# Performance work log

Hardware: AMD Instinct MI355X
Metric: run time of the kernel (lower is better)

## Reference

```python
import jax, jax.numpy as jnp
import numpy as np
import math

T, B = 512, 32
QD, SD, H, NH = 128, 256, 512, 8
NQ, NS, NSUB = 30000, 400, 8
DKEY = QD + 2 * SD      # 640
DVAL = 4 * SD + QD      # 1152
P = H + 2 * SD + QD     # 1152 (pred_in_feature)
DH = H // NH            # 64
NEG = -1e32


def _layernorm(x, g, b, eps=1e-5):
    mu = jnp.mean(x, axis=-1, keepdims=True)
    var = jnp.mean((x - mu) ** 2, axis=-1, keepdims=True)
    return (x - mu) * jax.lax.rsqrt(var + eps) * g + b


def setup_inputs() -> dict:
    key = jax.random.key(0)
    ks = iter(jax.random.split(key, 48))
    def nrm(shape, scale=0.05):
        return (scale * jax.random.normal(next(ks), shape)).astype(jnp.float32)
    inp = {}
    inp['ans'] = jax.random.randint(next(ks), (T, B), 1, 5, dtype=jnp.int32)
    inp['correct_ans'] = jax.random.randint(next(ks), (T, B), 1, 5, dtype=jnp.int32)
    inp['labels'] = jax.random.randint(next(ks), (T, B), 0, 2, dtype=jnp.int32)
    inp['mask'] = jnp.ones((T, B), jnp.float32)
    inp['q_ids'] = jax.random.randint(next(ks), (T, B), 0, NQ, dtype=jnp.int32)
    inp['subject_ids'] = jax.random.randint(next(ks), (T, B, NSUB), 0, NS, dtype=jnp.int32)
    inp['subject_mask'] = (jax.random.uniform(next(ks), (T, B, NSUB)) < 0.7).astype(jnp.float32)
    inp['Eq'] = nrm((NQ, QD)); inp['Es'] = nrm((NS, SD))
    inp['Ea'] = nrm((4, SD)); inp['El'] = nrm((2, SD))
    inp['Wq'] = nrm((H, DKEY)); inp['bq'] = jnp.zeros((H,), jnp.float32)
    inp['Wk'] = nrm((H, DKEY)); inp['bk'] = jnp.zeros((H,), jnp.float32)
    inp['Wv'] = nrm((H, DVAL)); inp['bv'] = jnp.zeros((H,), jnp.float32)
    inp['Wo'] = nrm((H, H)); inp['bo'] = jnp.zeros((H,), jnp.float32)
    inp['ln1_g'] = jnp.ones((H,), jnp.float32); inp['ln1_b'] = jnp.zeros((H,), jnp.float32)
    inp['W1'] = nrm((H, H)); inp['b1'] = jnp.zeros((H,), jnp.float32)
    inp['W2'] = nrm((H, H)); inp['b2'] = jnp.zeros((H,), jnp.float32)
    inp['ln2_g'] = jnp.ones((H,), jnp.float32); inp['ln2_b'] = jnp.zeros((H,), jnp.float32)
    inp['gammas'] = jnp.zeros((NH, 1, 1), jnp.float32)
    inp['L1W'] = nrm((P, P)); inp['L1b'] = jnp.zeros((P,), jnp.float32)
    inp['L2W'] = nrm((P, P)); inp['L2b'] = jnp.zeros((P,), jnp.float32)
    inp['OW'] = nrm((1, P)); inp['Ob'] = jnp.zeros((1,), jnp.float32)
    return inp


def _forward(ans, correct_ans, labels, q_ids, subject_ids,
             mask, subject_mask, Eq, Es, Ea, El,
             Wq, bq, Wk, bk, Wv, bv, Wo, bo, ln1_g, ln1_b,
             W1, b1, W2, b2, ln2_g, ln2_b, gammas,
             L1W, L1b, L2W, L2b, OW, Ob):
    m3 = mask[:, :, None]                                   # [T,B,1]
    subjects = jnp.sum(Es[subject_ids] * subject_mask[..., None], axis=2)   # [T,B,SD]
    questions = Eq[q_ids]                                   # [T,B,QD]
    ans_embed = Ea[ans - 1] * m3
    ca_embed = Ea[correct_ans - 1]
    lab_embed = El[labels] * m3
    query = jnp.concatenate([questions, subjects, ca_embed], axis=-1)       # [T,B,DKEY]
    value = jnp.concatenate([lab_embed, ans_embed, ca_embed, questions, subjects], axis=-1)  # [T,B,DVAL]
    # note: original applies q_linear to kk and k_linear to qq (qq==kk==query here); akt=True => no pos-embed
    q = (query @ Wq.T + bq).reshape(T, B, NH, DH).transpose(1, 2, 0, 3)     # [B,NH,T,DH]
    k = (query @ Wk.T + bk).reshape(T, B, NH, DH).transpose(1, 2, 0, 3)
    v = (value @ Wv.T + bv).reshape(T, B, NH, DH).transpose(1, 2, 0, 3)
    scores = jnp.einsum('bhqd,bhkd->bhqk', q, k) / math.sqrt(DH)            # [B,NH,T,T]
    scores = jnp.where(mask.T[:, None, None, :] == 0, NEG, scores)
    # exponential distance decay (Softplus-gamma), applied AFTER the key-pad fill as in the original
    idx = jnp.arange(T)
    pe = jnp.sqrt(jnp.abs(idx[None, :] - idx[:, None]).astype(jnp.float32)) # [T,T]
    total_effect = jnp.clip(jnp.exp(pe[None] * (-jax.nn.softplus(gammas))), 1e-5, 1e5)  # [NH,T,T]
    scores = scores * total_effect[None]
    causal_bad = jnp.triu(jnp.ones((T, T), bool))            # upper incl. diagonal is masked
    scores = jnp.where(causal_bad, NEG, scores)
    scores = jax.nn.softmax(scores, axis=-1)
    scores = scores.at[:, :, 0, :].set(0.0)                  # pad-zero first query row
    attn = jnp.einsum('bhqk,bhkd->bhqd', scores, v)
    concat = attn.transpose(2, 0, 1, 3).reshape(T, B, H)
    out = _layernorm(concat @ Wo.T + bo, ln1_g, ln1_b)
    ffn = jax.nn.relu(out @ W1.T + b1) @ W2.T + b2
    out = out + _layernorm(ffn, ln2_g, ln2_b)
    pred = jnp.concatenate([out, questions, subjects, ca_embed], axis=-1)   # [T,B,P]
    h = jax.nn.relu(pred @ L1W.T + L1b)
    h = jax.nn.relu(h @ L2W.T + L2b)
    logits = ((h + pred) @ OW.T + Ob)[..., 0]                # [T,B]
    y = labels.astype(jnp.float32)
    bce = jnp.maximum(logits, 0.0) - logits * y + jnp.log1p(jnp.exp(-jnp.abs(logits)))
    loss = jnp.mean(bce * mask) / jnp.mean(mask)
    return loss


def reference(ans, correct_ans, labels, mask, q_ids, subject_ids, subject_mask,
              Eq, Es, Ea, El, Wq, bq, Wk, bk, Wv, bv, Wo, bo, ln1_g, ln1_b,
              W1, b1, W2, b2, ln2_g, ln2_b, gammas, L1W, L1b, L2W, L2b, OW, Ob):
    return _forward(ans, correct_ans, labels, q_ids, subject_ids,
                    mask, subject_mask, Eq, Es, Ea, El,
                    Wq, bq, Wk, bk, Wv, bv, Wo, bo, ln1_g, ln1_b,
                    W1, b1, W2, b2, ln2_g, ln2_b, gammas,
                    L1W, L1b, L2W, L2b, OW, Ob)
```

## Files before the change

kernel.cpp:

```cpp
#include <hip/hip_runtime.h>
#include <math.h>

#define T_LEN 512
#define B_SZ  32
#define NHEAD 8
#define DHEAD 64
#define H_DIM 512
#define TBTOK 16384
#define P_DIM 1152

typedef unsigned short ushort_t;
typedef short short8 __attribute__((ext_vector_type(8)));
typedef float f32x4 __attribute__((ext_vector_type(4)));

__device__ __forceinline__ ushort_t f2bf(float f) {
    union { float f; unsigned int u; } v; v.f = f;
    unsigned int r = v.u + 0x7fffu + ((v.u >> 16) & 1u);
    return (ushort_t)(r >> 16);
}
__device__ __forceinline__ float bf2f(ushort_t h) {
    union { unsigned int u; float f; } v; v.u = ((unsigned int)h) << 16;
    return v.f;
}
__device__ __forceinline__ void gload_lds16(const void* g, void* l) {
    __builtin_amdgcn_global_load_lds(
        (const __attribute__((address_space(1))) void*)g,
        (__attribute__((address_space(3))) void*)l, 16, 0, 0);
}

__global__ __launch_bounds__(256) void convert_weights(
    const float* __restrict__ wq, const float* __restrict__ wk,
    const float* __restrict__ wv, const float* __restrict__ wo,
    const float* __restrict__ w1, const float* __restrict__ w2,
    const float* __restrict__ l1, const float* __restrict__ l2,
    ushort_t* __restrict__ dst)
{
    const unsigned int offs[9] = {0u, 327680u, 655360u, 1245184u, 1507328u,
                                  1769472u, 2031616u, 3358720u, 4685824u};
    unsigned int c = (blockIdx.x * 256 + threadIdx.x) * 4;
    const float* srcs[8] = {wq, wk, wv, wo, w1, w2, l1, l2};
    int s = 0;
#pragma unroll
    for (int i = 0; i < 7; i++) s += (c >= offs[i + 1]) ? 1 : 0;
    float4 v = *(const float4*)(srcs[s] + (c - offs[s]));
    ushort4 o;
    o.x = f2bf(v.x); o.y = f2bf(v.y); o.z = f2bf(v.z); o.w = f2bf(v.w);
    *(ushort4*)(dst + c) = o;
}

__global__ __launch_bounds__(256) void embed_kernel(
    const int* __restrict__ ans, const int* __restrict__ cans,
    const int* __restrict__ labels, const float* __restrict__ mask,
    const int* __restrict__ qids, const int* __restrict__ sids,
    const float* __restrict__ smask,
    const float* __restrict__ Eq, const float* __restrict__ Es,
    const float* __restrict__ Ea, const float* __restrict__ El,
    ushort_t* __restrict__ pred_bf, ushort_t* __restrict__ value_bf)
{
    int m = blockIdx.x;
    int tid = threadIdx.x;
    float mval = mask[m];
    int qid = qids[m];
    int a   = ans[m] - 1;
    int ca  = cans[m] - 1;
    int lb  = labels[m];
    ushort_t* pr = pred_bf  + (size_t)m * P_DIM;
    ushort_t* vr = value_bf + (size_t)m * P_DIM;

    if (tid < 128) {
        ushort_t qv = f2bf(Eq[(size_t)qid * 128 + tid]);
        pr[512 + tid] = qv;
        vr[768 + tid] = qv;
    }
    int d = tid;
    float s = 0.f;
#pragma unroll
    for (int j = 0; j < 8; j++) {
        int  sid = sids[m * 8 + j];
        float sm = smask[m * 8 + j];
        s += Es[(size_t)sid * 256 + d] * sm;
    }
    ushort_t sb = f2bf(s);
    pr[640 + d] = sb;
    vr[896 + d] = sb;
    ushort_t cab = f2bf(Ea[ca * 256 + d]);
    pr[896 + d] = cab;
    vr[512 + d] = cab;
    vr[256 + d] = f2bf(Ea[a * 256 + d] * mval);
    vr[0   + d] = f2bf(El[lb * 256 + d] * mval);
}

template<int MODE, bool RELU>
__global__ __launch_bounds__(256) void mgemm(
    const ushort_t* __restrict__ A, int lda,
    const ushort_t* __restrict__ W, int ldw,
    const float* __restrict__ bias, const float* __restrict__ bias2,
    ushort_t* __restrict__ Cb, ushort_t* __restrict__ Cb2, int ldc, int K,
    const float* __restrict__ OW, float* __restrict__ lg)
{
    __shared__ __align__(16) ushort_t As[128 * 32];
    __shared__ __align__(16) ushort_t Ws[128 * 32];
    __shared__ __align__(16) ushort_t et[4][32][72];

    const int m0 = blockIdx.x * 128;
    const int n0 = blockIdx.y * 128;
    const int tid  = threadIdx.x;
    const int wave = tid >> 6;
    const int lane = tid & 63;
    const int wm = wave & 1, wn = wave >> 1;

    f32x4 acc[4][4] = {};

    const int srow = lane >> 2;
    const int lchunk = ((((lane & 3) - ((srow >> 1) & 3)) & 3)) * 8;
    int arowA, arowB;
    if (MODE == 4) {
        int mA = m0 + wave * 32 + srow;
        int mB = mA + 16;
        arowA = ((mA & 511) << 5) + (mA >> 9);
        arowB = ((mB & 511) << 5) + (mB >> 9);
    } else {
        arowA = m0 + wave * 32 + srow;
        arowB = arowA + 16;
    }
    const ushort_t* Ag0 = A + (size_t)arowA * lda + lchunk;
    const ushort_t* Ag1 = A + (size_t)arowB * lda + lchunk;
    const ushort_t* Wg0 = W + (size_t)(n0 + wave * 32 + srow) * ldw + lchunk;
    const ushort_t* Wg1 = Wg0 + (size_t)16 * ldw;
    ushort_t* Al0 = &As[(wave * 32) * 32];
    ushort_t* Al1 = &As[(wave * 32 + 16) * 32];
    ushort_t* Wl0 = &Ws[(wave * 32) * 32];
    ushort_t* Wl1 = &Ws[(wave * 32 + 16) * 32];

    const int fr   = lane & 15;
    const int quad = lane >> 4;
    const int csw  = ((quad + ((fr >> 1) & 3)) & 3) * 8;

    for (int k0 = 0; k0 < K; k0 += 32) {
        gload_lds16(Ag0 + k0, Al0);
        gload_lds16(Ag1 + k0, Al1);
        gload_lds16(Wg0 + k0, Wl0);
        gload_lds16(Wg1 + k0, Wl1);
        __syncthreads();
        short8 af[4], wf[4];
#pragma unroll
        for (int i = 0; i < 4; i++)
            af[i] = *(const short8*)&As[(wm * 64 + i * 16 + fr) * 32 + csw];
#pragma unroll
        for (int j = 0; j < 4; j++)
            wf[j] = *(const short8*)&Ws[(wn * 64 + j * 16 + fr) * 32 + csw];
#pragma unroll
        for (int i = 0; i < 4; i++)
#pragma unroll
            for (int j = 0; j < 4; j++)
                acc[i][j] = __builtin_amdgcn_mfma_f32_16x16x32_bf16(
                    af[i], wf[j], acc[i][j], 0, 0, 0);
        __syncthreads();
    }

    if (MODE == 3) {
#pragma unroll
        for (int i = 0; i < 4; i++)
#pragma unroll
            for (int r = 0; r < 4; r++) {
                int row = m0 + wm * 64 + i * 16 + quad * 4 + r;
                float part = 0.f;
#pragma unroll
                for (int j = 0; j < 4; j++) {
                    int col = n0 + wn * 64 + j * 16 + fr;
                    float v = fmaxf(acc[i][j][r] + bias[col], 0.f);
                    part = fmaf(v, OW[col], part);
                }
                part += __shfl_xor(part, 1, 64);
                part += __shfl_xor(part, 2, 64);
                part += __shfl_xor(part, 4, 64);
                part += __shfl_xor(part, 8, 64);
                if (fr == 0) atomicAdd(&lg[row], part);
            }
        return;
    }

    const int nbase = n0 + wn * 64;
    bool side = (MODE == 5) && (nbase >= 512);
    const float* bp = side ? bias2 : bias;
    const int boff  = (MODE == 5) ? (nbase & 511) : nbase;
    const float scl = (MODE == 5 && !side) ? 0.125f : 1.f;

    const int sub8 = (lane & 7) * 8;
    const int grp  = lane >> 3;

#pragma unroll
    for (int hh = 0; hh < 2; hh++) {
        if (MODE == 4) {
#pragma unroll
            for (int i = 0; i < 4; i++)
#pragma unroll
                for (int r = 0; r < 4; r++) {
                    int rl = i * 16 + quad * 4 + r;
#pragma unroll
                    for (int j = 2 * hh; j < 2 * hh + 2; j++) {
                        int cl = j * 16 + fr;
                        float v = acc[i][j][r] + bp[boff + cl];
                        if (RELU) v = fmaxf(v, 0.f);
                        et[wave][cl - 32 * hh][rl] = f2bf(v);
                    }
                }
        } else {
#pragma unroll
            for (int i = 2 * hh; i < 2 * hh + 2; i++)
#pragma unroll
                for (int r = 0; r < 4; r++) {
                    int rl = i * 16 + quad * 4 + r;
#pragma unroll
                    for (int j = 0; j < 4; j++) {
                        int cl = j * 16 + fr;
                        float v = (acc[i][j][r] + bp[boff + cl]) * scl;
                        if (RELU) v = fmaxf(v, 0.f);
                        et[wave][rl - 32 * hh][cl] = f2bf(v);
                    }
                }
        }
#pragma unroll
        for (int rr = 0; rr < 4; rr++) {
            int rowl = rr * 8 + grp;
            short8 val = *(const short8*)&et[wave][rowl][sub8];
            if (MODE == 1) {
                int row = m0 + wm * 64 + 32 * hh + rowl;
                int col = nbase + sub8;
                *(short8*)&Cb[(size_t)row * ldc + col] = val;
            } else if (MODE == 5) {
                int row = m0 + wm * 64 + 32 * hh + rowl;
                int t = row >> 5, b = row & 31;
                int h = (nbase >> 6) & 7;
                ushort_t* base = side ? Cb2 : Cb;
                *(short8*)&base[(((size_t)(b * 8 + h)) << 15) + ((size_t)t << 6) + sub8] = val;
            } else {
                int m = m0 + wm * 64 + sub8;
                int b = m >> 9, t = m & 511;
                int h = nbase >> 6;
                int d = 32 * hh + rowl;
                *(short8*)&Cb[(((size_t)(b * 8 + h)) << 15) + ((size_t)d << 9) + t] = val;
            }
        }
    }
}

__global__ __launch_bounds__(256) void attn_mfma(
    const ushort_t* __restrict__ qb, const ushort_t* __restrict__ kb,
    const ushort_t* __restrict__ vtb, const float* __restrict__ mask,
    const float* __restrict__ gammas, ushort_t* __restrict__ attnc)
{
    __shared__ __align__(16) ushort_t kbuf[2][64 * 64];
    __shared__ __align__(16) ushort_t vbuf[2][64 * 64];
    __shared__ __align__(16) ushort_t ps[4][16][72];
    __shared__ float decayF[512];
    __shared__ float mneg[512];

    const int bh  = blockIdx.x;
    const int b   = bh >> 3;
    const int h   = bh & 7;
    const int qt0 = (7 - blockIdx.y) * 64;
    const int tid  = threadIdx.x;
    const int wave = tid >> 6;
    const int lane = tid & 63;
    const int fr   = lane & 15;
    const int quad = lane >> 4;

    {
        float g  = gammas[h];
        float sp = (g > 20.f) ? g : log1pf(expf(g));
        for (int i = tid; i < 512; i += 256) {
            decayF[i] = fmaxf(exp2f(-sp * 1.44269504f * sqrtf((float)i)), 1e-5f)
                        * 1.44269504f;
            mneg[i]   = (mask[(size_t)i * B_SZ + b] == 0.f) ? -1e32f : 0.f;
        }
    }

    const int qr0 = qt0 + wave * 16;
    const ushort_t* qbase = qb  + ((size_t)bh << 15);
    const ushort_t* kbase = kb  + ((size_t)bh << 15);
    const ushort_t* vbase = vtb + ((size_t)bh << 15);

    short8 af0 = *(const short8*)(qbase + (size_t)(qr0 + fr) * 64 + quad * 8);
    short8 af1 = *(const short8*)(qbase + (size_t)(qr0 + fr) * 64 + 32 + quad * 8);
    const short8 ones = {0x3F80, 0x3F80, 0x3F80, 0x3F80,
                         0x3F80, 0x3F80, 0x3F80, 0x3F80};

    const int rl0 = wave * 16 + (lane >> 3);
    const int rl1 = rl0 + 8;
    const int sc0 = (((lane & 7) - rl0) & 7) * 8;
    const int sc1 = (((lane & 7) - rl1) & 7) * 8;

    auto stage = [&](int kt, int bufi) {
        gload_lds16(kbase + (size_t)(kt + rl0) * 64 + sc0, &kbuf[bufi][(wave * 16) * 64]);
        gload_lds16(kbase + (size_t)(kt + rl1) * 64 + sc1, &kbuf[bufi][(wave * 16 + 8) * 64]);
        gload_lds16(vbase + (size_t)rl0 * T_LEN + kt + sc0, &vbuf[bufi][(wave * 16) * 64]);
        gload_lds16(vbase + (size_t)rl1 * T_LEN + kt + sc1, &vbuf[bufi][(wave * 16 + 8) * 64]);
    };
    auto frag = [&](const ushort_t* buf, int row, int lchunk) -> short8 {
        return *(const short8*)&buf[row * 64 + ((lchunk + row) & 7) * 8];
    };

    stage(0, 0);

    f32x4 o[4] = {};
    f32x4 lacc = {};
    int bufi = 0;

    for (int kt0 = 0; kt0 <= qt0; kt0 += 64) {
        __syncthreads();
        if (kt0 < qt0) stage(kt0 + 64, bufi ^ 1);
        const bool diag = (kt0 == qt0);
        const ushort_t* kb_ = kbuf[bufi];
        const ushort_t* vb_ = vbuf[bufi];

        f32x4 sacc[4] = {};
#pragma unroll
        for (int j = 0; j < 4; j++) {
            int row = j * 16 + fr;
            short8 k0 = frag(kb_, row, quad);
            short8 k1 = frag(kb_, row, quad + 4);
            sacc[j] = __builtin_amdgcn_mfma_f32_16x16x32_bf16(af0, k0, sacc[j], 0, 0, 0);
            sacc[j] = __builtin_amdgcn_mfma_f32_16x16x32_bf16(af1, k1, sacc[j], 0, 0, 0);
        }

#pragma unroll
        for (int j = 0; j < 4; j++) {
            int kg = kt0 + j * 16 + fr;
            float mn = mneg[kg];
            int qgb = qr0 + quad * 4;
            if (!diag) {
                int base = qgb - kg;
#pragma unroll
                for (int r = 0; r < 4; r++) {
                    float t = fmaf(sacc[j][r], decayF[base + r], mn);
                    union { float f; unsigned u; } cv; cv.f = exp2f(t);
                    ps[wave][quad * 4 + r][j * 16 + fr] = (ushort_t)(cv.u >> 16);
                }
            } else {
#pragma unroll
                for (int r = 0; r < 4; r++) {
                    int didx = qgb + r - kg;
                    float dec = decayF[didx > 0 ? didx : 0];
                    float t = fmaf(sacc[j][r], dec, mn);
                    if (didx <= 0) t = -1e32f;
                    union { float f; unsigned u; } cv; cv.f = exp2f(t);
                    ps[wave][quad * 4 + r][j * 16 + fr] = (ushort_t)(cv.u >> 16);
                }
            }
        }
        short8 pf0 = *(const short8*)&ps[wave][fr][quad * 8];
        short8 pf1 = *(const short8*)&ps[wave][fr][32 + quad * 8];
        lacc = __builtin_amdgcn_mfma_f32_16x16x32_bf16(pf0, ones, lacc, 0, 0, 0);
        lacc = __builtin_amdgcn_mfma_f32_16x16x32_bf16(pf1, ones, lacc, 0, 0, 0);
#pragma unroll
        for (int j2 = 0; j2 < 4; j2++) {
            int row = j2 * 16 + fr;
            short8 v0 = frag(vb_, row, quad);
            short8 v1 = frag(vb_, row, quad + 4);
            o[j2] = __builtin_amdgcn_mfma_f32_16x16x32_bf16(pf0, v0, o[j2], 0, 0, 0);
            o[j2] = __builtin_amdgcn_mfma_f32_16x16x32_bf16(pf1, v1, o[j2], 0, 0, 0);
        }
        bufi ^= 1;
    }

#pragma unroll
    for (int r = 0; r < 4; r++) {
        int qg = qr0 + quad * 4 + r;
        float linv = (qg == 0) ? 0.f : 1.f / lacc[r];
#pragma unroll
        for (int j2 = 0; j2 < 4; j2++)
            ps[wave][quad * 4 + r][j2 * 16 + fr] = f2bf(o[j2][r] * linv);
    }
    const int sub8 = (lane & 7) * 8;
    const int grp  = lane >> 3;
#pragma unroll
    for (int half = 0; half < 2; half++) {
        int rowl = half * 8 + grp;
        short8 val = *(const short8*)&ps[wave][rowl][sub8];
        int qg = qr0 + rowl;
        *(short8*)&attnc[((size_t)qg * B_SZ + b) * H_DIM + h * DHEAD + sub8] = val;
    }
}

__global__ __launch_bounds__(256) void ln1_kernel(
    const ushort_t* __restrict__ X, const float* __restrict__ g,
    const float* __restrict__ bta, float* __restrict__ Y,
    ushort_t* __restrict__ Yb)
{
    int m    = blockIdx.x * 4 + (threadIdx.x >> 6);
    int lane = threadIdx.x & 63;
    int c0   = lane * 8;
    const ushort_t* xr = X + (size_t)m * H_DIM + c0;
    float x[8];
    float s = 0.f, ss = 0.f;
    short8 xv = *(const short8*)xr;
#pragma unroll
    for (int i = 0; i < 8; i++) {
        x[i] = bf2f((ushort_t)xv[i]);
        s += x[i]; ss += x[i] * x[i];
    }
#pragma unroll
    for (int off = 32; off >= 1; off >>= 1) {
        s  += __shfl_xor(s,  off, 64);
        ss += __shfl_xor(ss, off, 64);
    }
    float mu  = s * (1.f / 512.f);
    float var = ss * (1.f / 512.f) - mu * mu;
    float rs  = rsqrtf(var + 1e-5f);
    float  yo[8];
    ushort_t yb[8];
#pragma unroll
    for (int i = 0; i < 8; i++) {
        float v = (x[i] - mu) * rs * g[c0 + i] + bta[c0 + i];
        yo[i] = v; yb[i] = f2bf(v);
    }
    *(float4*)(Y + (size_t)m * H_DIM + c0)     = *(float4*)&yo[0];
    *(float4*)(Y + (size_t)m * H_DIM + c0 + 4) = *(float4*)&yo[4];
    *(short8*)(Yb + (size_t)m * H_DIM + c0)    = *(short8*)&yb[0];
}

__global__ __launch_bounds__(256) void ln2_kernel(
    const ushort_t* __restrict__ X, const float* __restrict__ g,
    const float* __restrict__ bta, const float* __restrict__ res,
    ushort_t* __restrict__ pred_bf, const float* __restrict__ OW,
    float* __restrict__ lg)
{
    int m    = blockIdx.x * 4 + (threadIdx.x >> 6);
    int lane = threadIdx.x & 63;
    int c0   = lane * 8;
    const ushort_t* xr = X + (size_t)m * H_DIM + c0;
    float x[8];
    float s = 0.f, ss = 0.f;
    short8 xv = *(const short8*)xr;
#pragma unroll
    for (int i = 0; i < 8; i++) {
        x[i] = bf2f((ushort_t)xv[i]);
        s += x[i]; ss += x[i] * x[i];
    }
#pragma unroll
    for (int off = 32; off >= 1; off >>= 1) {
        s  += __shfl_xor(s,  off, 64);
        ss += __shfl_xor(ss, off, 64);
    }
    float mu  = s * (1.f / 512.f);
    float var = ss * (1.f / 512.f) - mu * mu;
    float rs  = rsqrtf(var + 1e-5f);
    float4 r0 = *(const float4*)(res + (size_t)m * H_DIM + c0);
    float4 r1 = *(const float4*)(res + (size_t)m * H_DIM + c0 + 4);
    float rr[8] = {r0.x, r0.y, r0.z, r0.w, r1.x, r1.y, r1.z, r1.w};
    ushort_t yb[8];
    float part = 0.f;
#pragma unroll
    for (int i = 0; i < 8; i++) {
        float v = (x[i] - mu) * rs * g[c0 + i] + bta[c0 + i] + rr[i];
        yb[i] = f2bf(v);
        part = fmaf(v, OW[c0 + i], part);
    }
    *(short8*)(pred_bf + (size_t)m * P_DIM + c0) = *(short8*)&yb[0];
#pragma unroll
    for (int off = 32; off >= 1; off >>= 1) part += __shfl_xor(part, off, 64);
    if (lane == 0) lg[m] += part;
}

__global__ __launch_bounds__(256) void predot_early(
    const ushort_t* __restrict__ pred_bf, const float* __restrict__ OW,
    const float* __restrict__ Ob, float* __restrict__ lg,
    float* __restrict__ accum)
{
    if (blockIdx.x == 0 && threadIdx.x < 2) accum[threadIdx.x] = 0.f;
    int m    = blockIdx.x * 4 + (threadIdx.x >> 6);
    int lane = threadIdx.x & 63;
    const ushort_t* pr = pred_bf + (size_t)m * P_DIM;
    float s = 0.f;
#pragma unroll 5
    for (int c = 512 + lane; c < P_DIM; c += 64)
        s = fmaf(bf2f(pr[c]), OW[c], s);
#pragma unroll
    for (int off = 32; off >= 1; off >>= 1) s += __shfl_xor(s, off, 64);
    if (lane == 0) lg[m] = s + Ob[0];
}

__global__ __launch_bounds__(256) void bce_kernel(
    const float* __restrict__ lg, const int* __restrict__ labels,
    const float* __restrict__ mask, float* __restrict__ accum)
{
    int m    = blockIdx.x * 256 + threadIdx.x;
    int lane = threadIdx.x & 63;
    float l  = lg[m];
    float y  = (float)labels[m];
    float mv = mask[m];
    float a  = (fmaxf(l, 0.f) - l * y + log1pf(expf(-fabsf(l)))) * mv;
#pragma unroll
    for (int off = 32; off >= 1; off >>= 1) {
        a  += __shfl_xor(a,  off, 64);
        mv += __shfl_xor(mv, off, 64);
    }
    if (lane == 0) {
        atomicAdd(accum,     a);
        atomicAdd(accum + 1, mv);
    }
}

__global__ void finalize_kernel(const float* __restrict__ accum, float* __restrict__ out)
{
    out[0] = accum[0] / accum[1];
}

extern "C" void kernel_launch(void* const* d_in, const int* in_sizes, int n_in,
                              void* d_out, int out_size, void* d_ws, size_t ws_size,
                              hipStream_t stream)
{
    (void)in_sizes; (void)n_in; (void)out_size;
    const int*   ans    = (const int*)  d_in[0];
    const int*   cans   = (const int*)  d_in[1];
    const int*   labels = (const int*)  d_in[2];
    const float* mask   = (const float*)d_in[3];
    const int*   qids   = (const int*)  d_in[4];
    const int*   sids   = (const int*)  d_in[5];
    const float* smask  = (const float*)d_in[6];
    const float* Eq     = (const float*)d_in[7];
    const float* Es     = (const float*)d_in[8];
    const float* Ea     = (const float*)d_in[9];
    const float* El     = (const float*)d_in[10];
    const float* Wq     = (const float*)d_in[11];
    const float* bq     = (const float*)d_in[12];
    const float* Wk     = (const float*)d_in[13];
    const float* bk     = (const float*)d_in[14];
    const float* Wv     = (const float*)d_in[15];
    const float* bv     = (const float*)d_in[16];
    const float* Wo     = (const float*)d_in[17];
    const float* bo     = (const float*)d_in[18];
    const float* ln1_g  = (const float*)d_in[19];
    const float* ln1_b  = (const float*)d_in[20];
    const float* W1     = (const float*)d_in[21];
    const float* b1     = (const float*)d_in[22];
    const float* W2     = (const float*)d_in[23];
    const float* b2     = (const float*)d_in[24];
    const float* ln2_g  = (const float*)d_in[25];
    const float* ln2_b  = (const float*)d_in[26];
    const float* gammas = (const float*)d_in[27];
    const float* L1W    = (const float*)d_in[28];
    const float* L1b    = (const float*)d_in[29];
    const float* L2W    = (const float*)d_in[30];
    const float* L2b    = (const float*)d_in[31];
    const float* OW     = (const float*)d_in[32];
    const float* Ob     = (const float*)d_in[33];
    float* out = (float*)d_out;

    const size_t U = (size_t)TBTOK * 64;
    if (ws_size < 42 * U * sizeof(float)) return;
    float* ws = (float*)d_ws;
    ushort_t* wtb      = (ushort_t*)(ws);
    ushort_t* pred_bf  = (ushort_t*)(ws + 3 * U);
    ushort_t* value_bf = (ushort_t*)(ws + 12 * U);
    ushort_t* qb       = (ushort_t*)(ws + 21 * U);
    ushort_t* kb       = (ushort_t*)(ws + 25 * U);
    ushort_t* vtb      = (ushort_t*)(ws + 29 * U);
    ushort_t* attnc_bf = (ushort_t*)(ws + 33 * U);
    ushort_t* x1_bf    = (ushort_t*)(ws + 12 * U);
    float*    out1     = ws + 16 * U;
    ushort_t* out1_bf  = (ushort_t*)(ws + 24 * U);
    ushort_t* f1_bf    = (ushort_t*)(ws + 28 * U);
    ushort_t* f2_bf    = (ushort_t*)(ws + 32 * U);
    ushort_t* h1_bf    = (ushort_t*)(ws + 12 * U);
    float*    lgits    = ws + 41 * U;
    float*    accum    = lgits + TBTOK;

    ushort_t* wqk_b = wtb + 0;
    ushort_t* wv_b  = wtb + 655360;
    ushort_t* wo_b  = wtb + 1245184;
    ushort_t* w1_b  = wtb + 1507328;
    ushort_t* w2_b  = wtb + 1769472;
    ushort_t* l1_b  = wtb + 2031616;
    ushort_t* l2_b  = wtb + 3358720;

    convert_weights<<<4576, 256, 0, stream>>>(Wq, Wk, Wv, Wo, W1, W2, L1W, L2W, wtb);
    embed_kernel<<<TBTOK, 256, 0, stream>>>(ans, cans, labels, mask, qids, sids,
                                            smask, Eq, Es, Ea, El, pred_bf, value_bf);
    predot_early<<<TBTOK/4, 256, 0, stream>>>(pred_bf, OW, Ob, lgits, accum);
    mgemm<5,false><<<dim3(TBTOK/128, 8), 256, 0, stream>>>(
        pred_bf + 512, P_DIM, wqk_b, 640, bq, bk, qb, kb, 0, 640, nullptr, nullptr);
    mgemm<4,false><<<dim3(TBTOK/128, 4), 256, 0, stream>>>(
        value_bf, P_DIM, wv_b, P_DIM, bv, nullptr, vtb, nullptr, 0, P_DIM, nullptr, nullptr);
    attn_mfma<<<dim3(B_SZ * NHEAD, 8), 256, 0, stream>>>(
        qb, kb, vtb, mask, gammas, attnc_bf);
    mgemm<1,false><<<dim3(TBTOK/128, 4), 256, 0, stream>>>(
        attnc_bf, H_DIM, wo_b, H_DIM, bo, nullptr, x1_bf, nullptr, H_DIM, H_DIM, nullptr, nullptr);
    ln1_kernel<<<TBTOK/4, 256, 0, stream>>>(x1_bf, ln1_g, ln1_b, out1, out1_bf);
    mgemm<1,true><<<dim3(TBTOK/128, 4), 256, 0, stream>>>(
        out1_bf, H_DIM, w1_b, H_DIM, b1, nullptr, f1_bf, nullptr, H_DIM, H_DIM, nullptr, nullptr);
    mgemm<1,false><<<dim3(TBTOK/128, 4), 256, 0, stream>>>(
        f1_bf, H_DIM, w2_b, H_DIM, b2, nullptr, f2_bf, nullptr, H_DIM, H_DIM, nullptr, nullptr);
    ln2_kernel<<<TBTOK/4, 256, 0, stream>>>(f2_bf, ln2_g, ln2_b, out1, pred_bf, OW, lgits);
    mgemm<1,true><<<dim3(TBTOK/128, 9), 256, 0, stream>>>(
        pred_bf, P_DIM, l1_b, P_DIM, L1b, nullptr, h1_bf, nullptr, P_DIM, P_DIM, nullptr, nullptr);
    mgemm<3,true><<<dim3(TBTOK/128, 9), 256, 0, stream>>>(
        h1_bf, P_DIM, l2_b, P_DIM, L2b, nullptr, nullptr, nullptr, 0, P_DIM, OW, lgits);
    bce_kernel<<<TBTOK/256, 256, 0, stream>>>(lgits, labels, mask, accum);
    finalize_kernel<<<1, 1, 0, stream>>>(accum, out);
}
```

Baseline: 485.0 us.

## Fuse pred logit dot into embed kernel and alias mgemm epilogue LDS

Removes the separate predot_early kernel by computing the pred columns 512..1151 dot with OW inside embed_kernel via wave shuffles and an LDS reduction, and moves accum zeroing into convert_weights. Separately, mgemm's epilogue staging buffer now aliases the A/W tile LDS and writes in four 16-row passes instead of two 32-row passes, cutting shared memory per block to raise occupancy. This saves one launch and a re-read of pred_bf, but adds a __syncthreads to the embed kernel and more epilogue iterations.

```diff
diff --git a/kernel.cpp b/kernel.cpp
--- a/kernel.cpp
+++ b/kernel.cpp
@@ -33,8 +33,9 @@
     const float* __restrict__ wv, const float* __restrict__ wo,
     const float* __restrict__ w1, const float* __restrict__ w2,
     const float* __restrict__ l1, const float* __restrict__ l2,
-    ushort_t* __restrict__ dst)
-{
+    ushort_t* __restrict__ dst, float* __restrict__ accum)
+{
+    if (blockIdx.x == 0 && threadIdx.x < 2) accum[threadIdx.x] = 0.f;
     const unsigned int offs[9] = {0u, 327680u, 655360u, 1245184u, 1507328u,
                                   1769472u, 2031616u, 3358720u, 4685824u};
     unsigned int c = (blockIdx.x * 256 + threadIdx.x) * 4;
@@ -55,8 +56,11 @@
     const float* __restrict__ smask,
     const float* __restrict__ Eq, const float* __restrict__ Es,
     const float* __restrict__ Ea, const float* __restrict__ El,
-    ushort_t* __restrict__ pred_bf, ushort_t* __restrict__ value_bf)
-{
+    ushort_t* __restrict__ pred_bf, ushort_t* __restrict__ value_bf,
+    const float* __restrict__ OW, const float* __restrict__ Ob,
+    float* __restrict__ lgits)
+{
+    __shared__ float red[4];
     int m = blockIdx.x;
     int tid = threadIdx.x;
     float mval = mask[m];
@@ -67,10 +71,12 @@
     ushort_t* pr = pred_bf  + (size_t)m * P_DIM;
     ushort_t* vr = value_bf + (size_t)m * P_DIM;
 
+    float part = 0.f;
     if (tid < 128) {
         ushort_t qv = f2bf(Eq[(size_t)qid * 128 + tid]);
         pr[512 + tid] = qv;
         vr[768 + tid] = qv;
+        part = bf2f(qv) * OW[512 + tid];
     }
     int d = tid;
     float s = 0.f;
@@ -88,6 +94,14 @@
     vr[512 + d] = cab;
     vr[256 + d] = f2bf(Ea[a * 256 + d] * mval);
     vr[0   + d] = f2bf(El[lb * 256 + d] * mval);
+
+    part = fmaf(bf2f(sb),  OW[640 + d], part);
+    part = fmaf(bf2f(cab), OW[896 + d], part);
+#pragma unroll
+    for (int off = 32; off >= 1; off >>= 1) part += __shfl_xor(part, off, 64);
+    if ((tid & 63) == 0) red[tid >> 6] = part;
+    __syncthreads();
+    if (tid == 0) lgits[m] = red[0] + red[1] + red[2] + red[3] + Ob[0];
 }
 
 template<int MODE, bool RELU>
@@ -98,9 +112,10 @@
     ushort_t* __restrict__ Cb, ushort_t* __restrict__ Cb2, int ldc, int K,
     const float* __restrict__ OW, float* __restrict__ lg)
 {
-    __shared__ __align__(16) ushort_t As[128 * 32];
-    __shared__ __align__(16) ushort_t Ws[128 * 32];
-    __shared__ __align__(16) ushort_t et[4][32][72];
+    __shared__ __align__(16) ushort_t smem[128 * 64];
+    ushort_t* As = smem;
+    ushort_t* Ws = smem + 128 * 32;
+    ushort_t* et = smem;
 
     const int m0 = blockIdx.x * 128;
     const int n0 = blockIdx.y * 128;
@@ -190,46 +205,40 @@
     const int grp  = lane >> 3;
 
 #pragma unroll
-    for (int hh = 0; hh < 2; hh++) {
+    for (int hh = 0; hh < 4; hh++) {
         if (MODE == 4) {
 #pragma unroll
             for (int i = 0; i < 4; i++)
 #pragma unroll
                 for (int r = 0; r < 4; r++) {
                     int rl = i * 16 + quad * 4 + r;
-#pragma unroll
-                    for (int j = 2 * hh; j < 2 * hh + 2; j++) {
-                        int cl = j * 16 + fr;
-                        float v = acc[i][j][r] + bp[boff + cl];
-                        if (RELU) v = fmaxf(v, 0.f);
-                        et[wave][cl - 32 * hh][rl] = f2bf(v);
-                    }
+                    float v = acc[i][hh][r] + bp[boff + hh * 16 + fr];
+                    if (RELU) v = fmaxf(v, 0.f);
+                    et[(wave * 16 + fr) * 72 + rl] = f2bf(v);
                 }
         } else {
 #pragma unroll
-            for (int i = 2 * hh; i < 2 * hh + 2; i++)
-#pragma unroll
-                for (int r = 0; r < 4; r++) {
-                    int rl = i * 16 + quad * 4 + r;
-#pragma unroll
-                    for (int j = 0; j < 4; j++) {
-                        int cl = j * 16 + fr;
-                        float v = (acc[i][j][r] + bp[boff + cl]) * scl;
-                        if (RELU) v = fmaxf(v, 0.f);
-                        et[wave][rl - 32 * hh][cl] = f2bf(v);
-                    }
+            for (int r = 0; r < 4; r++) {
+                int rl = quad * 4 + r;
+#pragma unroll
+                for (int j = 0; j < 4; j++) {
+                    int cl = j * 16 + fr;
+                    float v = (acc[hh][j][r] + bp[boff + cl]) * scl;
+                    if (RELU) v = fmaxf(v, 0.f);
+                    et[(wave * 16 + rl) * 72 + cl] = f2bf(v);
                 }
+            }
         }
 #pragma unroll
-        for (int rr = 0; rr < 4; rr++) {
+        for (int rr = 0; rr < 2; rr++) {
             int rowl = rr * 8 + grp;
-            short8 val = *(const short8*)&et[wave][rowl][sub8];
+            short8 val = *(const short8*)&et[(wave * 16 + rowl) * 72 + sub8];
             if (MODE == 1) {
-                int row = m0 + wm * 64 + 32 * hh + rowl;
+                int row = m0 + wm * 64 + 16 * hh + rowl;
                 int col = nbase + sub8;
                 *(short8*)&Cb[(size_t)row * ldc + col] = val;
             } else if (MODE == 5) {
-                int row = m0 + wm * 64 + 32 * hh + rowl;
+                int row = m0 + wm * 64 + 16 * hh + rowl;
                 int t = row >> 5, b = row & 31;
                 int h = (nbase >> 6) & 7;
                 ushort_t* base = side ? Cb2 : Cb;
@@ -238,7 +247,7 @@
                 int m = m0 + wm * 64 + sub8;
                 int b = m >> 9, t = m & 511;
                 int h = nbase >> 6;
-                int d = 32 * hh + rowl;
+                int d = 16 * hh + rowl;
                 *(short8*)&Cb[(((size_t)(b * 8 + h)) << 15) + ((size_t)d << 9) + t] = val;
             }
         }
@@ -461,24 +470,6 @@
 #pragma unroll
     for (int off = 32; off >= 1; off >>= 1) part += __shfl_xor(part, off, 64);
     if (lane == 0) lg[m] += part;
-}
-
-__global__ __launch_bounds__(256) void predot_early(
-    const ushort_t* __restrict__ pred_bf, const float* __restrict__ OW,
-    const float* __restrict__ Ob, float* __restrict__ lg,
-    float* __restrict__ accum)
-{
-    if (blockIdx.x == 0 && threadIdx.x < 2) accum[threadIdx.x] = 0.f;
-    int m    = blockIdx.x * 4 + (threadIdx.x >> 6);
-    int lane = threadIdx.x & 63;
-    const ushort_t* pr = pred_bf + (size_t)m * P_DIM;
-    float s = 0.f;
-#pragma unroll 5
-    for (int c = 512 + lane; c < P_DIM; c += 64)
-        s = fmaf(bf2f(pr[c]), OW[c], s);
-#pragma unroll
-    for (int off = 32; off >= 1; off >>= 1) s += __shfl_xor(s, off, 64);
-    if (lane == 0) lg[m] = s + Ob[0];
 }
 
 __global__ __launch_bounds__(256) void bce_kernel(
@@ -575,10 +566,11 @@
     ushort_t* l1_b  = wtb + 2031616;
     ushort_t* l2_b  = wtb + 3358720;
 
-    convert_weights<<<4576, 256, 0, stream>>>(Wq, Wk, Wv, Wo, W1, W2, L1W, L2W, wtb);
+    convert_weights<<<4576, 256, 0, stream>>>(Wq, Wk, Wv, Wo, W1, W2, L1W, L2W,
+                                              wtb, accum);
     embed_kernel<<<TBTOK, 256, 0, stream>>>(ans, cans, labels, mask, qids, sids,
-                                            smask, Eq, Es, Ea, El, pred_bf, value_bf);
-    predot_early<<<TBTOK/4, 256, 0, stream>>>(pred_bf, OW, Ob, lgits, accum);
+                                            smask, Eq, Es, Ea, El, pred_bf, value_bf,
+                                            OW, Ob, lgits);
     mgemm<5,false><<<dim3(TBTOK/128, 8), 256, 0, stream>>>(
         pred_bf + 512, P_DIM, wqk_b, 640, bq, bk, qb, kb, 0, 640, nullptr, nullptr);
     mgemm<4,false><<<dim3(TBTOK/128, 4), 256, 0, stream>>>(
```

New measurement: 497.7 us. 1.03x slower.
